# Kernel tuning notes

Hardware: AMD Instinct MI355X
Metric: run time of the kernel (lower is better)

## Reference

```python
import math
import jax, jax.numpy as jnp
import numpy as np

B, S, H, M, E = 4, 4096, 1024, 1024, 16
CAPACITY_FACTOR = 2.0
ROUTE_SCALE = 1.0


def setup_inputs() -> dict:
    key = jax.random.key(0)
    ks = jax.random.split(key, 8)
    return {
        "hidden_states": jax.random.normal(ks[0], (B, S, H), dtype=jnp.float32),
        "hidden_states_unmodulated": jax.random.normal(ks[1], (B, S, H), dtype=jnp.float32),
        "timestep": jax.random.normal(ks[2], (B, H), dtype=jnp.float32),
        "gate_w": jax.random.normal(ks[3], (2 * H, E), dtype=jnp.float32) * 0.02,
        "gate_up_proj": jax.random.normal(ks[4], (E, H, 2 * M), dtype=jnp.float32) * 0.02,
        "down_proj": jax.random.normal(ks[5], (E, M, H), dtype=jnp.float32) * 0.02,
        "shared_gate_up_w": jax.random.normal(ks[6], (H, 2 * M), dtype=jnp.float32) * 0.02,
        "shared_down_w": jax.random.normal(ks[7], (M, H), dtype=jnp.float32) * 0.02,
    }


def reference(hidden_states, hidden_states_unmodulated, timestep, gate_w,
              gate_up_proj, down_proj, shared_gate_up_w, shared_down_w):
    b, s, h = hidden_states.shape
    e = gate_up_proj.shape[0]
    capacity = max(1, math.ceil(CAPACITY_FACTOR * s / e))  # static per shapes

    # --- router ---
    t = jnp.broadcast_to(timestep[:, None, :], (b, s, h))
    router_input = jnp.concatenate([t, hidden_states_unmodulated], axis=-1)  # [b,s,2h]
    logits = router_input @ gate_w                                           # [b,s,e]
    scores = jax.nn.sigmoid(logits.astype(jnp.float32)).astype(logits.dtype)
    affinity = jnp.swapaxes(scores, 1, 2)                                    # [b,e,s]

    # --- expert-choice top-k ---
    gating, top_idx = jax.lax.top_k(affinity, capacity)                      # [b,e,cap]
    offsets = (jnp.arange(b) * s)[:, None, None]
    gidx = jnp.swapaxes(offsets + top_idx, 0, 1).reshape(-1)                 # [e*b*cap]
    gflat = jnp.swapaxes(gating, 0, 1).reshape(-1)

    # normalize per-token scores over experts that picked the token
    sums = jnp.zeros(b * s, dtype=gflat.dtype).at[gidx].add(gflat)
    gflat = gflat / (sums[gidx] + 1e-12) * ROUTE_SCALE

    # --- dispatch + grouped SwiGLU experts ---
    x_flat = hidden_states.reshape(b * s, h)
    routed = x_flat[gidx].reshape(e, b * capacity, h)
    gu = jnp.einsum('eth,ehf->etf', routed, gate_up_proj)                    # [e,t,2m]
    g, u = jnp.split(gu, 2, axis=-1)
    expert_out = jnp.einsum('etm,emh->eth', jax.nn.silu(g) * u, down_proj)
    expert_out = expert_out.reshape(e * b * capacity, h)
    expert_out = (expert_out.astype(jnp.float32) *
                  gflat.astype(jnp.float32)[:, None]).astype(hidden_states.dtype)

    # --- shared expert (SwiGLUProj order: hidden * silu(gate)) ---
    hgu = hidden_states @ shared_gate_up_w                                   # [b,s,2m]
    hs_, hg = jnp.split(hgu, 2, axis=-1)
    shared = (hs_ * jax.nn.silu(hg)) @ shared_down_w                         # [b,s,h]

    # --- scatter combine ---
    out = shared.reshape(b * s, h).at[gidx].add(expert_out)
    return out.reshape(b, s, h)
```

## Files before the change

kernel.cpp:

```cpp
#include <hip/hip_runtime.h>
#include <math.h>

#define Bb 4
#define Ss 4096
#define Hh 1024
#define Mm 1024
#define Ee 16
#define CAPk 512

typedef unsigned short u16;
typedef __attribute__((ext_vector_type(8))) short short8;
typedef __attribute__((ext_vector_type(4))) float floatx4;
typedef __attribute__((ext_vector_type(4))) unsigned short ushort4v;

__device__ __forceinline__ float silu_f(float x) {
    return x / (1.0f + expf(-x));
}

__device__ __forceinline__ u16 f2b(float x) {
    union { float f; unsigned u; } v; v.f = x;
    unsigned r = (v.u + 0x7fffu + ((v.u >> 16) & 1u)) >> 16;
    return (u16)r;
}

__device__ __forceinline__ void gl_lds16(const void* g, void* l) {
    __builtin_amdgcn_global_load_lds((const __attribute__((address_space(1))) void*)g,
                                     (__attribute__((address_space(3))) void*)l, 16, 0, 0);
}


__global__ __launch_bounds__(256)
void router_scores(const float* __restrict__ hsu,
                   const float* __restrict__ gate_w,
                   const float* __restrict__ timestep,
                   float* __restrict__ scores) {
    __shared__ float Xs[64 * 64];
    __shared__ float Gs[64 * 16];
    const int t = threadIdx.x;
    const int row0 = blockIdx.x * 64;
    const int b = row0 >> 12;
    const int wave = t >> 6, lane = t & 63;
    const int e0 = wave * 4;
    const float* gw2 = gate_w + (size_t)Hh * Ee;

    float tl0 = 0.f, tl1 = 0.f, tl2 = 0.f, tl3 = 0.f;
    {
        const float* tsrow = timestep + (size_t)b * Hh;
#pragma unroll
        for (int j = 0; j < 16; ++j) {
            int h = lane + 64 * j;
            float tv = tsrow[h];
            const float* gw = gate_w + (size_t)h * Ee + e0;
            tl0 += tv * gw[0]; tl1 += tv * gw[1]; tl2 += tv * gw[2]; tl3 += tv * gw[3];
        }
#pragma unroll
        for (int off = 32; off; off >>= 1) {
            tl0 += __shfl_xor(tl0, off); tl1 += __shfl_xor(tl1, off);
            tl2 += __shfl_xor(tl2, off); tl3 += __shfl_xor(tl3, off);
        }
    }

    float acc0 = 0.f, acc1 = 0.f, acc2 = 0.f, acc3 = 0.f;

    for (int k0 = 0; k0 < Hh; k0 += 64) {
        __syncthreads();
#pragma unroll
        for (int r = 0; r < 4; ++r) {
            int tok = r * 16 + (t >> 4);
            int cslot = t & 15;
            int g = cslot ^ (tok & 15);
            const float* src = hsu + (size_t)(row0 + tok) * Hh + k0 + g * 4;
            char* dst = (char*)Xs + r * 4096 + wave * 1024;
            gl_lds16(src, dst);
        }
        {
            const float* src = gw2 + (size_t)k0 * Ee + t * 4;
            char* dst = (char*)Gs + wave * 1024;
            gl_lds16(src, dst);
        }
        __syncthreads();
#pragma unroll
        for (int kk = 0; kk < 64; kk += 4) {
            int slot = (kk >> 2) ^ (lane & 15);
            float4 a = *(const float4*)&Xs[lane * 64 + slot * 4];
            float4 g0 = *(const float4*)&Gs[(kk + 0) * Ee + e0];
            float4 g1 = *(const float4*)&Gs[(kk + 1) * Ee + e0];
            float4 g2 = *(const float4*)&Gs[(kk + 2) * Ee + e0];
            float4 g3 = *(const float4*)&Gs[(kk + 3) * Ee + e0];
            acc0 += a.x * g0.x; acc0 += a.y * g1.x; acc0 += a.z * g2.x; acc0 += a.w * g3.x;
            acc1 += a.x * g0.y; acc1 += a.y * g1.y; acc1 += a.z * g2.y; acc1 += a.w * g3.y;
            acc2 += a.x * g0.z; acc2 += a.y * g1.z; acc2 += a.z * g2.z; acc2 += a.w * g3.z;
            acc3 += a.x * g0.w; acc3 += a.y * g1.w; acc3 += a.z * g2.w; acc3 += a.w * g3.w;
        }
    }
    const int s = (row0 + lane) & (Ss - 1);
    float l0 = acc0 + tl0;
    float l1 = acc1 + tl1;
    float l2 = acc2 + tl2;
    float l3 = acc3 + tl3;
    scores[((size_t)(b * Ee + e0 + 0)) * Ss + s] = 1.f / (1.f + expf(-l0));
    scores[((size_t)(b * Ee + e0 + 1)) * Ss + s] = 1.f / (1.f + expf(-l1));
    scores[((size_t)(b * Ee + e0 + 2)) * Ss + s] = 1.f / (1.f + expf(-l2));
    scores[((size_t)(b * Ee + e0 + 3)) * Ss + s] = 1.f / (1.f + expf(-l3));
}

__global__ __launch_bounds__(256)
void topk_kernel(const float* __restrict__ scores,
                 int* __restrict__ sel_idx,
                 float* __restrict__ sel_gate) {
    const int be = blockIdx.x;
    const float* sc = scores + (size_t)be * Ss;
    const int t = threadIdx.x;
    const int lane = t & 63, w = t >> 6;
    __shared__ unsigned hist[256];
    __shared__ unsigned wtot[4];
    __shared__ unsigned sh_prefix;
    __shared__ int sh_need;
    __shared__ unsigned cnt_gt;

    unsigned vu[16];
#pragma unroll
    for (int i = 0; i < 16; ++i) vu[i] = __float_as_uint(sc[t * 16 + i]);

    unsigned prefix = 0;
    int need = CAPk;
    for (int pass = 0; pass < 4; ++pass) {
        const int shift = 24 - 8 * pass;
        hist[t] = 0;
        __syncthreads();
#pragma unroll
        for (int i = 0; i < 16; ++i) {
            unsigned u = vu[i];
            bool ok = (pass == 0) || ((u >> (shift + 8)) == prefix);
            if (ok) atomicAdd(&hist[(u >> shift) & 255u], 1u);
        }
        __syncthreads();
        unsigned hval = hist[t];
        unsigned s = hval;
#pragma unroll
        for (int d = 1; d < 64; d <<= 1) {
            unsigned o = __shfl_down(s, d);
            if (lane + d < 64) s += o;
        }
        if (lane == 0) wtot[w] = s;
        __syncthreads();
#pragma unroll
        for (int w2 = 0; w2 < 4; ++w2)
            if (w2 > w) s += wtot[w2];
        unsigned Snext = s - hval;
        if (s >= (unsigned)need && Snext < (unsigned)need) {
            sh_prefix = (prefix << 8) | (unsigned)t;
            sh_need = need - (int)Snext;
        }
        __syncthreads();
        prefix = sh_prefix;
        need = sh_need;
        __syncthreads();
    }
    const unsigned T = prefix;
    const int need_eq = need;
    const unsigned ngt = (unsigned)(CAPk - need_eq);

    int myeq = 0;
#pragma unroll
    for (int i = 0; i < 16; ++i) myeq += (vu[i] == T) ? 1 : 0;
    unsigned e = (unsigned)myeq;
#pragma unroll
    for (int d = 1; d < 64; d <<= 1) {
        unsigned o = __shfl_up(e, d);
        if (lane >= d) e += o;
    }
    if (lane == 63) wtot[w] = e;
    if (t == 0) cnt_gt = 0;
    __syncthreads();
    unsigned eqr = e - (unsigned)myeq;
#pragma unroll
    for (int w2 = 0; w2 < 4; ++w2)
        if (w2 < w) eqr += wtot[w2];
#pragma unroll
    for (int i = 0; i < 16; ++i) {
        unsigned u = vu[i];
        int s = t * 16 + i;
        if (u > T) {
            unsigned slot = atomicAdd(&cnt_gt, 1u);
            sel_idx[(size_t)be * CAPk + slot] = s;
            sel_gate[(size_t)be * CAPk + slot] = __uint_as_float(u);
        } else if (u == T) {
            if ((int)eqr < need_eq) {
                unsigned slot = ngt + eqr;
                sel_idx[(size_t)be * CAPk + slot] = s;
                sel_gate[(size_t)be * CAPk + slot] = __uint_as_float(u);
            }
            eqr++;
        }
    }
}

__global__ void zero2_kernel(float* __restrict__ sums, int* __restrict__ cnt) {
    int i = blockIdx.x * 256 + threadIdx.x;
    sums[i] = 0.f;
    cnt[i] = 0;
}

__global__ void accum_kernel(const int* __restrict__ sel_idx,
                             const float* __restrict__ sel_gate,
                             float* __restrict__ sums) {
    int g = blockIdx.x * 256 + threadIdx.x;
    int be = g / CAPk;
    int b = be >> 4;
    atomicAdd(&sums[b * Ss + sel_idx[g]], sel_gate[g]);
}

__global__ void finalize_kernel(const int* __restrict__ sel_idx,
                                const float* __restrict__ sel_gate,
                                const float* __restrict__ sums,
                                int* __restrict__ slot_token,
                                float* __restrict__ slot_w,
                                int* __restrict__ cnt,
                                int* __restrict__ inv) {
    int g = blockIdx.x * 256 + threadIdx.x;
    int be = g / CAPk, c = g % CAPk;
    int b = be >> 4, e = be & 15;
    int token = b * Ss + sel_idx[g];
    float wv = sel_gate[g] / (sums[token] + 1e-12f);
    int o = (e * Bb + b) * CAPk + c;
    slot_token[o] = token;
    slot_w[o] = wv;
    int pos = atomicAdd(&cnt[token], 1);
    inv[(size_t)token * 16 + pos] = o;
}

__global__ __launch_bounds__(256)
void combine_kernel(const int* __restrict__ cnt, const int* __restrict__ inv,
                    const float* __restrict__ eo, float* __restrict__ out) {
    const int token = blockIdx.x;
    const int k = cnt[token];
    if (k == 0) return;
    const int col = threadIdx.x * 4;
    const size_t rowoff = (size_t)token * 1024 + col;
    float4 acc = *(const float4*)(out + rowoff);
    for (int j = 0; j < k; ++j) {
        int slot = inv[token * 16 + j];
        float4 v = *(const float4*)(eo + (size_t)slot * 1024 + col);
        acc.x += v.x; acc.y += v.y; acc.z += v.z; acc.w += v.w;
    }
    *(float4*)(out + rowoff) = acc;
}


__global__ __launch_bounds__(256)
void convert_bf16(const float* __restrict__ src, u16* __restrict__ dst) {
    int i = (blockIdx.x * 256 + threadIdx.x) * 4;
    float4 v = *(const float4*)(src + i);
    ushort4v o = { f2b(v.x), f2b(v.y), f2b(v.z), f2b(v.w) };
    *(ushort4v*)(dst + i) = o;
}

__global__ __launch_bounds__(256)
void transpose_bf16(const float* __restrict__ W, u16* __restrict__ Wt,
                    int N, size_t zsrc, size_t zdst) {
    __shared__ float tile[64][65];
    int n0 = blockIdx.x * 64, k0 = blockIdx.y * 64, z = blockIdx.z;
    const float* Ws = W + (size_t)z * zsrc;
    u16* Wd = Wt + (size_t)z * zdst;
    int t = threadIdx.x;
    int lr = t >> 4, lc = (t & 15) * 4;
#pragma unroll
    for (int i = 0; i < 4; ++i) {
        float4 v = *(const float4*)&Ws[(size_t)(k0 + lr + i * 16) * N + n0 + lc];
        tile[lr + i * 16][lc + 0] = v.x;
        tile[lr + i * 16][lc + 1] = v.y;
        tile[lr + i * 16][lc + 2] = v.z;
        tile[lr + i * 16][lc + 3] = v.w;
    }
    __syncthreads();
    int on = t >> 2;
    int ok0 = (t & 3) * 16;
    u16 buf[16];
#pragma unroll
    for (int j = 0; j < 16; ++j) buf[j] = f2b(tile[ok0 + j][on]);
    u16* dp = &Wd[(size_t)(n0 + on) * 1024 + k0 + ok0];
    *(short8*)(dp) = *(short8*)&buf[0];
    *(short8*)(dp + 8) = *(short8*)&buf[8];
}


__device__ __forceinline__ void stage_tile(const u16* __restrict__ grow, int k0,
                                           u16* lds, int t) {
#pragma unroll
    for (int r = 0; r < 4; ++r) {
        int o = (r * 256 + t) * 16;
        int m = o >> 7;
        int c = ((o >> 4) & 7) ^ (m & 7);
        const u16* src = grow + (size_t)m * 1024 + k0 + c * 8;
        u16* dst = lds + ((r * 4096 + (t >> 6) * 1024) >> 1);
        gl_lds16(src, dst);
    }
}

__device__ __forceinline__ void stage_rows(const u16* __restrict__ A, const int* rid,
                                           int k0, u16* lds, int t) {
#pragma unroll
    for (int r = 0; r < 4; ++r) {
        int m = (t >> 3) + 32 * r;
        int c = (t & 7) ^ (m & 7);
        const u16* src = A + (size_t)rid[r] * 1024 + k0 + c * 8;
        u16* dst = lds + ((r * 4096 + (t >> 6) * 1024) >> 1);
        gl_lds16(src, dst);
    }
}

template <bool SILU_FIRST, bool GATHER>
__global__ __launch_bounds__(256, 2)
void gemm1_mfma(const u16* __restrict__ A, int a_row0, int zstride,
                const u16* __restrict__ W1t, u16* __restrict__ act,
                const int* __restrict__ slot_token, int e_base) {
    __shared__ u16 lA[128 * 64];
    __shared__ u16 lB1[128 * 64];
    __shared__ u16 lB2[128 * 64];
    const int t = threadIdx.x;
    const int n0 = blockIdx.x * 128;
    const int bm0 = blockIdx.y * 128;
    const int z = blockIdx.z;
    const int zb = z * zstride;
    const u16* B1row = W1t + ((size_t)z * 2048 + n0) * 1024;
    const u16* B2row = B1row + (size_t)1024 * 1024;
    const int lane = t & 63;
    const int wv = t >> 6, wm = wv & 1, wn = wv >> 1;
    const int quad = lane >> 4, l15 = lane & 15;

    int rid[4];
#pragma unroll
    for (int r = 0; r < 4; ++r) {
        int m = (t >> 3) + 32 * r;
        rid[r] = GATHER ? slot_token[(e_base + z) * (Bb * CAPk) + bm0 + m]
                        : (a_row0 + zb + bm0 + m);
    }

    floatx4 zero4 = {0.f, 0.f, 0.f, 0.f};
    floatx4 acc1[4][4], acc2[4][4];
#pragma unroll
    for (int i = 0; i < 4; ++i)
#pragma unroll
        for (int j = 0; j < 4; ++j) { acc1[i][j] = zero4; acc2[i][j] = zero4; }

    for (int k0 = 0; k0 < 1024; k0 += 64) {
        __syncthreads();
        stage_rows(A, rid, k0, lA, t);
        stage_tile(B1row, k0, lB1, t);
        stage_tile(B2row, k0, lB2, t);
        __syncthreads();
#pragma unroll
        for (int kc = 0; kc < 2; ++kc) {
            short8 af[4], bf1[4], bf2[4];
#pragma unroll
            for (int mi = 0; mi < 4; ++mi) {
                int m = wm * 64 + mi * 16 + l15;
                int off = m * 64 + (((kc * 4 + quad) ^ (m & 7)) * 8);
                af[mi] = *(const short8*)&lA[off];
            }
#pragma unroll
            for (int ni = 0; ni < 4; ++ni) {
                int n = wn * 64 + ni * 16 + l15;
                int off = n * 64 + (((kc * 4 + quad) ^ (n & 7)) * 8);
                bf1[ni] = *(const short8*)&lB1[off];
                bf2[ni] = *(const short8*)&lB2[off];
            }
#pragma unroll
            for (int mi = 0; mi < 4; ++mi)
#pragma unroll
                for (int ni = 0; ni < 4; ++ni) {
                    acc1[mi][ni] = __builtin_amdgcn_mfma_f32_16x16x32_bf16(af[mi], bf1[ni], acc1[mi][ni], 0, 0, 0);
                    acc2[mi][ni] = __builtin_amdgcn_mfma_f32_16x16x32_bf16(af[mi], bf2[ni], acc2[mi][ni], 0, 0, 0);
                }
        }
    }
#pragma unroll
    for (int mi = 0; mi < 4; ++mi)
#pragma unroll
        for (int ni = 0; ni < 4; ++ni)
#pragma unroll
            for (int r = 0; r < 4; ++r) {
                int m = wm * 64 + mi * 16 + quad * 4 + r;
                int n = wn * 64 + ni * 16 + l15;
                float c1 = acc1[mi][ni][r], c2 = acc2[mi][ni][r];
                float v = SILU_FIRST ? silu_f(c1) * c2 : c1 * silu_f(c2);
                act[(size_t)(zb + bm0 + m) * 1024 + n0 + n] = f2b(v);
            }
}

template <int MODE>
__global__ __launch_bounds__(256, 2)
void gemm2_mfma(const u16* __restrict__ A, int zstride,
                const u16* __restrict__ W2t,
                const int* __restrict__ slot_token, const float* __restrict__ slot_w,
                float* __restrict__ out, int out_row0, int e_base) {
    __shared__ u16 lA[128 * 64];
    __shared__ u16 lB[128 * 64];
    __shared__ int s_tok[(MODE == 1) ? 128 : 1];
    __shared__ float s_w[(MODE == 1 || MODE == 2) ? 128 : 1];
    const int t = threadIdx.x;
    const int n0 = blockIdx.x * 128;
    const int bm0 = blockIdx.y * 128;
    const int z = blockIdx.z;
    const int zb = z * zstride;
    const u16* Arow = A + (size_t)(zb + bm0) * 1024;
    const u16* Brow = W2t + ((size_t)z * 1024 + n0) * 1024;
    const int lane = t & 63;
    const int wv = t >> 6, wm = wv & 1, wn = wv >> 1;
    const int quad = lane >> 4, l15 = lane & 15;

    if ((MODE == 1 || MODE == 2) && t < 128) {
        int gi = (e_base + z) * (Bb * CAPk) + bm0 + t;
        if (MODE == 1) s_tok[t] = slot_token[gi];
        s_w[t] = slot_w[gi];
    }

    floatx4 zero4 = {0.f, 0.f, 0.f, 0.f};
    floatx4 acc[4][4];
#pragma unroll
    for (int i = 0; i < 4; ++i)
#pragma unroll
        for (int j = 0; j < 4; ++j) acc[i][j] = zero4;

    for (int k0 = 0; k0 < 1024; k0 += 64) {
        __syncthreads();
        stage_tile(Arow, k0, lA, t);
        stage_tile(Brow, k0, lB, t);
        __syncthreads();
#pragma unroll
        for (int kc = 0; kc < 2; ++kc) {
            short8 af[4], bf[4];
#pragma unroll
            for (int mi = 0; mi < 4; ++mi) {
                int m = wm * 64 + mi * 16 + l15;
                int off = m * 64 + (((kc * 4 + quad) ^ (m & 7)) * 8);
                af[mi] = *(const short8*)&lA[off];
            }
#pragma unroll
            for (int ni = 0; ni < 4; ++ni) {
                int n = wn * 64 + ni * 16 + l15;
                int off = n * 64 + (((kc * 4 + quad) ^ (n & 7)) * 8);
                bf[ni] = *(const short8*)&lB[off];
            }
#pragma unroll
            for (int mi = 0; mi < 4; ++mi)
#pragma unroll
                for (int ni = 0; ni < 4; ++ni)
                    acc[mi][ni] = __builtin_amdgcn_mfma_f32_16x16x32_bf16(af[mi], bf[ni], acc[mi][ni], 0, 0, 0);
        }
    }
#pragma unroll
    for (int mi = 0; mi < 4; ++mi)
#pragma unroll
        for (int ni = 0; ni < 4; ++ni)
#pragma unroll
            for (int r = 0; r < 4; ++r) {
                int m = wm * 64 + mi * 16 + quad * 4 + r;
                int n = wn * 64 + ni * 16 + l15;
                float c = acc[mi][ni][r];
                if (MODE == 1) {
                    atomicAdd(&out[(size_t)s_tok[m] * 1024 + n0 + n], c * s_w[m]);
                } else if (MODE == 2) {
                    out[((size_t)((e_base + z) * (Bb * CAPk) + bm0 + m)) * 1024 + n0 + n] = c * s_w[m];
                } else {
                    out[(size_t)(out_row0 + bm0 + m) * 1024 + n0 + n] = c;
                }
            }
}


extern "C" void kernel_launch(void* const* d_in, const int* in_sizes, int n_in,
                              void* d_out, int out_size, void* d_ws, size_t ws_size,
                              hipStream_t stream) {
    const float* hidden   = (const float*)d_in[0];
    const float* hsu      = (const float*)d_in[1];
    const float* timestep = (const float*)d_in[2];
    const float* gate_w   = (const float*)d_in[3];
    const float* gate_up  = (const float*)d_in[4];
    const float* down     = (const float*)d_in[5];
    const float* sh_gu    = (const float*)d_in[6];
    const float* sh_dn    = (const float*)d_in[7];
    float* out = (float*)d_out;

    char* p = (char*)d_ws;
    auto alloc = [&](size_t bytes) { char* r = p; p += (bytes + 255) & ~(size_t)255; return r; };
    float* scores    = (float*)alloc((size_t)Bb * Ee * Ss * 4);
    int*   sel_idx   = (int*)  alloc((size_t)Bb * Ee * CAPk * 4);
    float* sel_gate  = (float*)alloc((size_t)Bb * Ee * CAPk * 4);
    float* sums      = (float*)alloc((size_t)Bb * Ss * 4);
    int*   slot_token= (int*)  alloc((size_t)Ee * Bb * CAPk * 4);
    float* slot_w    = (float*)alloc((size_t)Ee * Bb * CAPk * 4);
    int*   cnt       = (int*)  alloc((size_t)Bb * Ss * 4);
    int*   inv       = (int*)  alloc((size_t)Bb * Ss * 16 * 4);
    u16*   Xb        = (u16*)  alloc((size_t)16384 * 1024 * 2);
    char* phase = p;
    long long avail = (long long)((char*)d_ws + ws_size - phase);
    if (avail < 0) avail = 0;

    const long long eo_bytes     = (long long)32768 * 1024 * 4;
    const long long per_e        = ((long long)2048 * 1024 + 1024 * 1024 +
                                    (long long)2048 * 1024) * 2;
    const long long shared_fixed = ((long long)2048 * 1024 + 1024 * 1024) * 2;

    convert_bf16<<<16384, 256, 0, stream>>>(hidden, Xb);
    router_scores<<<(Bb * Ss) / 64, 256, 0, stream>>>(hsu, gate_w, timestep, scores);
    topk_kernel<<<Bb * Ee, 256, 0, stream>>>(scores, sel_idx, sel_gate);
    zero2_kernel<<<(Bb * Ss) / 256, 256, 0, stream>>>(sums, cnt);
    accum_kernel<<<(Bb * Ee * CAPk) / 256, 256, 0, stream>>>(sel_idx, sel_gate, sums);
    finalize_kernel<<<(Bb * Ee * CAPk) / 256, 256, 0, stream>>>(sel_idx, sel_gate, sums,
                                                                slot_token, slot_w, cnt, inv);

    long long min_shared = shared_fixed + (long long)128 * 2048;
    bool use_eo = (avail >= eo_bytes + (per_e > min_shared ? per_e : min_shared));

    if (use_eo) {
        float* eo = (float*)phase;
        char* ph2 = phase + eo_bytes;
        long long avail2 = avail - eo_bytes;

        {
            int g = (int)(avail2 / per_e);
            if (g < 1) g = 1;
            if (g > Ee) g = Ee;
            u16* Wt1r = (u16*)ph2;
            u16* Wt2r = Wt1r + (size_t)g * 2048 * 1024;
            u16* actR = Wt2r + (size_t)g * 1024 * 1024;

            for (int e0 = 0; e0 < Ee; e0 += g) {
                int cg = Ee - e0; if (cg > g) cg = g;
                transpose_bf16<<<dim3(32, 16, cg), 256, 0, stream>>>(
                    gate_up + (size_t)e0 * 2097152, Wt1r, 2048, 2097152, 2097152);
                transpose_bf16<<<dim3(16, 16, cg), 256, 0, stream>>>(
                    down + (size_t)e0 * 1048576, Wt2r, 1024, 1048576, 1048576);
                gemm1_mfma<true, true><<<dim3(8, 16, cg), 256, 0, stream>>>(
                    Xb, 0, 2048, Wt1r, actR, slot_token, e0);
                gemm2_mfma<2><<<dim3(8, 16, cg), 256, 0, stream>>>(
                    actR, 2048, Wt2r, slot_token, slot_w, eo, 0, e0);
            }
        }

        {
            u16* Wt1s = (u16*)ph2;
            u16* Wt2s = Wt1s + (size_t)2048 * 1024;
            u16* actS = Wt2s + (size_t)1024 * 1024;
            long long room = (avail2 - shared_fixed) / 2048;
            room &= ~127LL;
            int R = (int)(room > 16384 ? 16384 : room);
            if (R < 128) R = 128;

            transpose_bf16<<<dim3(32, 16, 1), 256, 0, stream>>>(sh_gu, Wt1s, 2048, 0, 0);
            transpose_bf16<<<dim3(16, 16, 1), 256, 0, stream>>>(sh_dn, Wt2s, 1024, 0, 0);
            for (int r0 = 0; r0 < Bb * Ss; r0 += R) {
                int cur = Bb * Ss - r0; if (cur > R) cur = R;
                gemm1_mfma<false, false><<<dim3(8, cur / 128, 1), 256, 0, stream>>>(
                    Xb, r0, 0, Wt1s, actS, nullptr, 0);
                gemm2_mfma<0><<<dim3(8, cur / 128, 1), 256, 0, stream>>>(
                    actS, 0, Wt2s, nullptr, nullptr, out, r0, 0);
            }
        }

        combine_kernel<<<Bb * Ss, 256, 0, stream>>>(cnt, inv, eo, out);
    } else {
        {
            u16* Wt1s = (u16*)phase;
            u16* Wt2s = Wt1s + (size_t)2048 * 1024;
            u16* actS = Wt2s + (size_t)1024 * 1024;
            long long room = (avail - shared_fixed) / 2048;
            room &= ~127LL;
            int R = (int)(room > 16384 ? 16384 : room);
            if (R < 128) R = 128;

            transpose_bf16<<<dim3(32, 16, 1), 256, 0, stream>>>(sh_gu, Wt1s, 2048, 0, 0);
            transpose_bf16<<<dim3(16, 16, 1), 256, 0, stream>>>(sh_dn, Wt2s, 1024, 0, 0);
            for (int r0 = 0; r0 < Bb * Ss; r0 += R) {
                int cur = Bb * Ss - r0; if (cur > R) cur = R;
                gemm1_mfma<false, false><<<dim3(8, cur / 128, 1), 256, 0, stream>>>(
                    Xb, r0, 0, Wt1s, actS, nullptr, 0);
                gemm2_mfma<0><<<dim3(8, cur / 128, 1), 256, 0, stream>>>(
                    actS, 0, Wt2s, nullptr, nullptr, out, r0, 0);
            }
        }
        {
            int g = (int)(avail / per_e);
            if (g < 1) g = 1;
            if (g > Ee) g = Ee;
            u16* Wt1r = (u16*)phase;
            u16* Wt2r = Wt1r + (size_t)g * 2048 * 1024;
            u16* actR = Wt2r + (size_t)g * 1024 * 1024;

            for (int e0 = 0; e0 < Ee; e0 += g) {
                int cg = Ee - e0; if (cg > g) cg = g;
                transpose_bf16<<<dim3(32, 16, cg), 256, 0, stream>>>(
                    gate_up + (size_t)e0 * 2097152, Wt1r, 2048, 2097152, 2097152);
                transpose_bf16<<<dim3(16, 16, cg), 256, 0, stream>>>(
                    down + (size_t)e0 * 1048576, Wt2r, 1024, 1048576, 1048576);
                gemm1_mfma<true, true><<<dim3(8, 16, cg), 256, 0, stream>>>(
                    Xb, 0, 2048, Wt1r, actR, slot_token, e0);
                gemm2_mfma<1><<<dim3(8, 16, cg), 256, 0, stream>>>(
                    actR, 2048, Wt2r, slot_token, slot_w, out, 0, e0);
            }
        }
    }
}
```

Baseline: 803.3 us.

## Use 512-thread GEMM blocks and fold sums/cnt zeroing into a 1024-thread top-k

The two MFMA GEMM kernels keep the same 128x128 block tile but now run with 8 waves instead of 4. Each wave computes a 64x32 sub-tile, LDS staging is spread over 512 threads, and launch bounds are raised to (512,4) to get more waves resident for latency hiding. The top-k selection kernel now uses 1024 threads holding 4 scores each, and it zeroes the sums and counts buffers itself, so the separate zero kernel launch is gone. The tighter register budget from launch_bounds(512,4) risks register spilling in gemm1, which carries two accumulator sets. Each wave also does less MFMA work per LDS fragment it loads, which lowers data reuse.

Result: slower. 821.2 us (+2.2%).

```diff
diff --git a/kernel.cpp b/kernel.cpp
--- a/kernel.cpp
+++ b/kernel.cpp
@@ -104,53 +104,59 @@
     scores[((size_t)(b * Ee + e0 + 3)) * Ss + s] = 1.f / (1.f + expf(-l3));
 }
 
-__global__ __launch_bounds__(256)
+__global__ __launch_bounds__(1024)
 void topk_kernel(const float* __restrict__ scores,
                  int* __restrict__ sel_idx,
-                 float* __restrict__ sel_gate) {
+                 float* __restrict__ sel_gate,
+                 float* __restrict__ sums,
+                 int* __restrict__ cnt) {
     const int be = blockIdx.x;
     const float* sc = scores + (size_t)be * Ss;
     const int t = threadIdx.x;
     const int lane = t & 63, w = t >> 6;
     __shared__ unsigned hist[256];
-    __shared__ unsigned wtot[4];
+    __shared__ unsigned wtot[16];
     __shared__ unsigned sh_prefix;
     __shared__ int sh_need;
     __shared__ unsigned cnt_gt;
 
-    unsigned vu[16];
-#pragma unroll
-    for (int i = 0; i < 16; ++i) vu[i] = __float_as_uint(sc[t * 16 + i]);
+    if (t < 256) { sums[be * 256 + t] = 0.f; cnt[be * 256 + t] = 0; }
+
+    unsigned vu[4];
+#pragma unroll
+    for (int i = 0; i < 4; ++i) vu[i] = __float_as_uint(sc[t * 4 + i]);
 
     unsigned prefix = 0;
     int need = CAPk;
     for (int pass = 0; pass < 4; ++pass) {
         const int shift = 24 - 8 * pass;
-        hist[t] = 0;
-        __syncthreads();
-#pragma unroll
-        for (int i = 0; i < 16; ++i) {
+        if (t < 256) hist[t] = 0;
+        __syncthreads();
+#pragma unroll
+        for (int i = 0; i < 4; ++i) {
             unsigned u = vu[i];
             bool ok = (pass == 0) || ((u >> (shift + 8)) == prefix);
             if (ok) atomicAdd(&hist[(u >> shift) & 255u], 1u);
         }
         __syncthreads();
-        unsigned hval = hist[t];
+        unsigned hval = (t < 256) ? hist[t] : 0u;
         unsigned s = hval;
 #pragma unroll
         for (int d = 1; d < 64; d <<= 1) {
             unsigned o = __shfl_down(s, d);
             if (lane + d < 64) s += o;
         }
-        if (lane == 0) wtot[w] = s;
-        __syncthreads();
-#pragma unroll
-        for (int w2 = 0; w2 < 4; ++w2)
-            if (w2 > w) s += wtot[w2];
-        unsigned Snext = s - hval;
-        if (s >= (unsigned)need && Snext < (unsigned)need) {
-            sh_prefix = (prefix << 8) | (unsigned)t;
-            sh_need = need - (int)Snext;
+        if (lane == 0 && w < 4) wtot[w] = s;
+        __syncthreads();
+        if (t < 256) {
+#pragma unroll
+            for (int w2 = 0; w2 < 4; ++w2)
+                if (w2 > w) s += wtot[w2];
+            unsigned Snext = s - hval;
+            if (s >= (unsigned)need && Snext < (unsigned)need) {
+                sh_prefix = (prefix << 8) | (unsigned)t;
+                sh_need = need - (int)Snext;
+            }
         }
         __syncthreads();
         prefix = sh_prefix;
@@ -163,7 +169,7 @@
 
     int myeq = 0;
 #pragma unroll
-    for (int i = 0; i < 16; ++i) myeq += (vu[i] == T) ? 1 : 0;
+    for (int i = 0; i < 4; ++i) myeq += (vu[i] == T) ? 1 : 0;
     unsigned e = (unsigned)myeq;
 #pragma unroll
     for (int d = 1; d < 64; d <<= 1) {
@@ -175,12 +181,12 @@
     __syncthreads();
     unsigned eqr = e - (unsigned)myeq;
 #pragma unroll
-    for (int w2 = 0; w2 < 4; ++w2)
+    for (int w2 = 0; w2 < 16; ++w2)
         if (w2 < w) eqr += wtot[w2];
 #pragma unroll
-    for (int i = 0; i < 16; ++i) {
+    for (int i = 0; i < 4; ++i) {
         unsigned u = vu[i];
-        int s = t * 16 + i;
+        int s = t * 4 + i;
         if (u > T) {
             unsigned slot = atomicAdd(&cnt_gt, 1u);
             sel_idx[(size_t)be * CAPk + slot] = s;
@@ -194,12 +200,6 @@
             eqr++;
         }
     }
-}
-
-__global__ void zero2_kernel(float* __restrict__ sums, int* __restrict__ cnt) {
-    int i = blockIdx.x * 256 + threadIdx.x;
-    sums[i] = 0.f;
-    cnt[i] = 0;
 }
 
 __global__ void accum_kernel(const int* __restrict__ sel_idx,
@@ -285,33 +285,34 @@
 }
 
 
-__device__ __forceinline__ void stage_tile(const u16* __restrict__ grow, int k0,
-                                           u16* lds, int t) {
-#pragma unroll
-    for (int r = 0; r < 4; ++r) {
-        int o = (r * 256 + t) * 16;
-        int m = o >> 7;
-        int c = ((o >> 4) & 7) ^ (m & 7);
+__device__ __forceinline__ void stage_tile512(const u16* __restrict__ grow, int k0,
+                                              u16* lds, int t) {
+#pragma unroll
+    for (int r = 0; r < 2; ++r) {
+        int ci = r * 512 + t;
+        int m = ci >> 3;
+        int c = (ci & 7) ^ (m & 7);
         const u16* src = grow + (size_t)m * 1024 + k0 + c * 8;
-        u16* dst = lds + ((r * 4096 + (t >> 6) * 1024) >> 1);
+        u16* dst = lds + ((r * 8192 + (t >> 6) * 1024) >> 1);
         gl_lds16(src, dst);
     }
 }
 
-__device__ __forceinline__ void stage_rows(const u16* __restrict__ A, const int* rid,
-                                           int k0, u16* lds, int t) {
-#pragma unroll
-    for (int r = 0; r < 4; ++r) {
-        int m = (t >> 3) + 32 * r;
-        int c = (t & 7) ^ (m & 7);
+__device__ __forceinline__ void stage_rows512(const u16* __restrict__ A, const int* rid,
+                                              int k0, u16* lds, int t) {
+#pragma unroll
+    for (int r = 0; r < 2; ++r) {
+        int ci = r * 512 + t;
+        int m = ci >> 3;
+        int c = (ci & 7) ^ (m & 7);
         const u16* src = A + (size_t)rid[r] * 1024 + k0 + c * 8;
-        u16* dst = lds + ((r * 4096 + (t >> 6) * 1024) >> 1);
+        u16* dst = lds + ((r * 8192 + (t >> 6) * 1024) >> 1);
         gl_lds16(src, dst);
     }
 }
 
 template <bool SILU_FIRST, bool GATHER>
-__global__ __launch_bounds__(256, 2)
+__global__ __launch_bounds__(512, 4)
 void gemm1_mfma(const u16* __restrict__ A, int a_row0, int zstride,
                 const u16* __restrict__ W1t, u16* __restrict__ act,
                 const int* __restrict__ slot_token, int e_base) {
@@ -326,33 +327,34 @@
     const u16* B1row = W1t + ((size_t)z * 2048 + n0) * 1024;
     const u16* B2row = B1row + (size_t)1024 * 1024;
     const int lane = t & 63;
-    const int wv = t >> 6, wm = wv & 1, wn = wv >> 1;
+    const int wv = t >> 6;
+    const int wm = wv & 1, wn = wv >> 1;
     const int quad = lane >> 4, l15 = lane & 15;
 
-    int rid[4];
-#pragma unroll
-    for (int r = 0; r < 4; ++r) {
-        int m = (t >> 3) + 32 * r;
+    int rid[2];
+#pragma unroll
+    for (int r = 0; r < 2; ++r) {
+        int m = (t >> 3) + 64 * r;
         rid[r] = GATHER ? slot_token[(e_base + z) * (Bb * CAPk) + bm0 + m]
                         : (a_row0 + zb + bm0 + m);
     }
 
     floatx4 zero4 = {0.f, 0.f, 0.f, 0.f};
-    floatx4 acc1[4][4], acc2[4][4];
+    floatx4 acc1[4][2], acc2[4][2];
 #pragma unroll
     for (int i = 0; i < 4; ++i)
 #pragma unroll
-        for (int j = 0; j < 4; ++j) { acc1[i][j] = zero4; acc2[i][j] = zero4; }
+        for (int j = 0; j < 2; ++j) { acc1[i][j] = zero4; acc2[i][j] = zero4; }
 
     for (int k0 = 0; k0 < 1024; k0 += 64) {
         __syncthreads();
-        stage_rows(A, rid, k0, lA, t);
-        stage_tile(B1row, k0, lB1, t);
-        stage_tile(B2row, k0, lB2, t);
+        stage_rows512(A, rid, k0, lA, t);
+        stage_tile512(B1row, k0, lB1, t);
+        stage_tile512(B2row, k0, lB2, t);
         __syncthreads();
 #pragma unroll
         for (int kc = 0; kc < 2; ++kc) {
-            short8 af[4], bf1[4], bf2[4];
+            short8 af[4], bf1[2], bf2[2];
 #pragma unroll
             for (int mi = 0; mi < 4; ++mi) {
                 int m = wm * 64 + mi * 16 + l15;
@@ -360,8 +362,8 @@
                 af[mi] = *(const short8*)&lA[off];
             }
 #pragma unroll
-            for (int ni = 0; ni < 4; ++ni) {
-                int n = wn * 64 + ni * 16 + l15;
+            for (int ni = 0; ni < 2; ++ni) {
+                int n = wn * 32 + ni * 16 + l15;
                 int off = n * 64 + (((kc * 4 + quad) ^ (n & 7)) * 8);
                 bf1[ni] = *(const short8*)&lB1[off];
                 bf2[ni] = *(const short8*)&lB2[off];
@@ -369,7 +371,7 @@
 #pragma unroll
             for (int mi = 0; mi < 4; ++mi)
 #pragma unroll
-                for (int ni = 0; ni < 4; ++ni) {
+                for (int ni = 0; ni < 2; ++ni) {
                     acc1[mi][ni] = __builtin_amdgcn_mfma_f32_16x16x32_bf16(af[mi], bf1[ni], acc1[mi][ni], 0, 0, 0);
                     acc2[mi][ni] = __builtin_amdgcn_mfma_f32_16x16x32_bf16(af[mi], bf2[ni], acc2[mi][ni], 0, 0, 0);
                 }
@@ -378,11 +380,11 @@
 #pragma unroll
     for (int mi = 0; mi < 4; ++mi)
 #pragma unroll
-        for (int ni = 0; ni < 4; ++ni)
+        for (int ni = 0; ni < 2; ++ni)
 #pragma unroll
             for (int r = 0; r < 4; ++r) {
                 int m = wm * 64 + mi * 16 + quad * 4 + r;
-                int n = wn * 64 + ni * 16 + l15;
+                int n = wn * 32 + ni * 16 + l15;
                 float c1 = acc1[mi][ni][r], c2 = acc2[mi][ni][r];
                 float v = SILU_FIRST ? silu_f(c1) * c2 : c1 * silu_f(c2);
                 act[(size_t)(zb + bm0 + m) * 1024 + n0 + n] = f2b(v);
@@ -390,7 +392,7 @@
 }
 
 template <int MODE>
-__global__ __launch_bounds__(256, 2)
+__global__ __launch_bounds__(512, 4)
 void gemm2_mfma(const u16* __restrict__ A, int zstride,
                 const u16* __restrict__ W2t,
                 const int* __restrict__ slot_token, const float* __restrict__ slot_w,
@@ -407,7 +409,8 @@
     const u16* Arow = A + (size_t)(zb + bm0) * 1024;
     const u16* Brow = W2t + ((size_t)z * 1024 + n0) * 1024;
     const int lane = t & 63;
-    const int wv = t >> 6, wm = wv & 1, wn = wv >> 1;
+    const int wv = t >> 6;
+    const int wm = wv & 1, wn = wv >> 1;
     const int quad = lane >> 4, l15 = lane & 15;
 
     if ((MODE == 1 || MODE == 2) && t < 128) {
@@ -417,20 +420,20 @@
     }
 
     floatx4 zero4 = {0.f, 0.f, 0.f, 0.f};
-    floatx4 acc[4][4];
+    floatx4 acc[4][2];
 #pragma unroll
     for (int i = 0; i < 4; ++i)
 #pragma unroll
-        for (int j = 0; j < 4; ++j) acc[i][j] = zero4;
+        for (int j = 0; j < 2; ++j) acc[i][j] = zero4;
 
     for (int k0 = 0; k0 < 1024; k0 += 64) {
         __syncthreads();
-        stage_tile(Arow, k0, lA, t);
-        stage_tile(Brow, k0, lB, t);
+        stage_tile512(Arow, k0, lA, t);
+        stage_tile512(Brow, k0, lB, t);
         __syncthreads();
 #pragma unroll
         for (int kc = 0; kc < 2; ++kc) {
-            short8 af[4], bf[4];
+            short8 af[4], bf[2];
 #pragma unroll
             for (int mi = 0; mi < 4; ++mi) {
                 int m = wm * 64 + mi * 16 + l15;
@@ -438,26 +441,26 @@
                 af[mi] = *(const short8*)&lA[off];
             }
 #pragma unroll
-            for (int ni = 0; ni < 4; ++ni) {
-                int n = wn * 64 + ni * 16 + l15;
+            for (int ni = 0; ni < 2; ++ni) {
+                int n = wn * 32 + ni * 16 + l15;
                 int off = n * 64 + (((kc * 4 + quad) ^ (n & 7)) * 8);
                 bf[ni] = *(const short8*)&lB[off];
             }
 #pragma unroll
             for (int mi = 0; mi < 4; ++mi)
 #pragma unroll
-                for (int ni = 0; ni < 4; ++ni)
+                for (int ni = 0; ni < 2; ++ni)
                     acc[mi][ni] = __builtin_amdgcn_mfma_f32_16x16x32_bf16(af[mi], bf[ni], acc[mi][ni], 0, 0, 0);
         }
     }
 #pragma unroll
     for (int mi = 0; mi < 4; ++mi)
 #pragma unroll
-        for (int ni = 0; ni < 4; ++ni)
+        for (int ni = 0; ni < 2; ++ni)
 #pragma unroll
             for (int r = 0; r < 4; ++r) {
                 int m = wm * 64 + mi * 16 + quad * 4 + r;
-                int n = wn * 64 + ni * 16 + l15;
+                int n = wn * 32 + ni * 16 + l15;
                 float c = acc[mi][ni][r];
                 if (MODE == 1) {
                     atomicAdd(&out[(size_t)s_tok[m] * 1024 + n0 + n], c * s_w[m]);
@@ -505,8 +508,7 @@
 
     convert_bf16<<<16384, 256, 0, stream>>>(hidden, Xb);
     router_scores<<<(Bb * Ss) / 64, 256, 0, stream>>>(hsu, gate_w, timestep, scores);
-    topk_kernel<<<Bb * Ee, 256, 0, stream>>>(scores, sel_idx, sel_gate);
-    zero2_kernel<<<(Bb * Ss) / 256, 256, 0, stream>>>(sums, cnt);
+    topk_kernel<<<Bb * Ee, 1024, 0, stream>>>(scores, sel_idx, sel_gate, sums, cnt);
     accum_kernel<<<(Bb * Ee * CAPk) / 256, 256, 0, stream>>>(sel_idx, sel_gate, sums);
     finalize_kernel<<<(Bb * Ee * CAPk) / 256, 256, 0, stream>>>(sel_idx, sel_gate, sums,
                                                                 slot_token, slot_w, cnt, inv);
@@ -533,9 +535,9 @@
                     gate_up + (size_t)e0 * 2097152, Wt1r, 2048, 2097152, 2097152);
                 transpose_bf16<<<dim3(16, 16, cg), 256, 0, stream>>>(
                     down + (size_t)e0 * 1048576, Wt2r, 1024, 1048576, 1048576);
-                gemm1_mfma<true, true><<<dim3(8, 16, cg), 256, 0, stream>>>(
+                gemm1_mfma<true, true><<<dim3(8, 16, cg), 512, 0, stream>>>(
                     Xb, 0, 2048, Wt1r, actR, slot_token, e0);
-                gemm2_mfma<2><<<dim3(8, 16, cg), 256, 0, stream>>>(
+                gemm2_mfma<2><<<dim3(8, 16, cg), 512, 0, stream>>>(
                     actR, 2048, Wt2r, slot_token, slot_w, eo, 0, e0);
             }
         }
@@ -553,9 +555,9 @@
             transpose_bf16<<<dim3(16, 16, 1), 256, 0, stream>>>(sh_dn, Wt2s, 1024, 0, 0);
             for (int r0 = 0; r0 < Bb * Ss; r0 += R) {
                 int cur = Bb * Ss - r0; if (cur > R) cur = R;
-                gemm1_mfma<false, false><<<dim3(8, cur / 128, 1), 256, 0, stream>>>(
+                gemm1_mfma<false, false><<<dim3(8, cur / 128, 1), 512, 0, stream>>>(
                     Xb, r0, 0, Wt1s, actS, nullptr, 0);
-                gemm2_mfma<0><<<dim3(8, cur / 128, 1), 256, 0, stream>>>(
+                gemm2_mfma<0><<<dim3(8, cur / 128, 1), 512, 0, stream>>>(
                     actS, 0, Wt2s, nullptr, nullptr, out, r0, 0);
             }
         }
@@ -575,9 +577,9 @@
             transpose_bf16<<<dim3(16, 16, 1), 256, 0, stream>>>(sh_dn, Wt2s, 1024, 0, 0);
             for (int r0 = 0; r0 < Bb * Ss; r0 += R) {
                 int cur = Bb * Ss - r0; if (cur > R) cur = R;
-                gemm1_mfma<false, false><<<dim3(8, cur / 128, 1), 256, 0, stream>>>(
+                gemm1_mfma<false, false><<<dim3(8, cur / 128, 1), 512, 0, stream>>>(
                     Xb, r0, 0, Wt1s, actS, nullptr, 0);
-                gemm2_mfma<0><<<dim3(8, cur / 128, 1), 256, 0, stream>>>(
+                gemm2_mfma<0><<<dim3(8, cur / 128, 1), 512, 0, stream>>>(
                     actS, 0, Wt2s, nullptr, nullptr, out, r0, 0);
             }
         }
@@ -595,9 +597,9 @@
                     gate_up + (size_t)e0 * 2097152, Wt1r, 2048, 2097152, 2097152);
                 transpose_bf16<<<dim3(16, 16, cg), 256, 0, stream>>>(
                     down + (size_t)e0 * 1048576, Wt2r, 1024, 1048576, 1048576);
-                gemm1_mfma<true, true><<<dim3(8, 16, cg), 256, 0, stream>>>(
+                gemm1_mfma<true, true><<<dim3(8, 16, cg), 512, 0, stream>>>(
                     Xb, 0, 2048, Wt1r, actR, slot_token, e0);
-                gemm2_mfma<1><<<dim3(8, 16, cg), 256, 0, stream>>>(
+                gemm2_mfma<1><<<dim3(8, 16, cg), 512, 0, stream>>>(
                     actR, 2048, Wt2r, slot_token, slot_w, out, 0, e0);
             }
         }
```
